# Performance work log

Hardware: AMD Instinct MI355X
Metric: run time of the kernel (lower is better)

Reference implementation:

```python
import jax, jax.numpy as jnp
import numpy as np

W1 = 1.0
W2 = 1.0


def setup_inputs() -> dict:
    key = jax.random.key(0)
    k1, k2 = jax.random.split(key)
    points1 = jax.random.normal(k1, (8, 4096, 3), dtype=jnp.float32)
    points2 = jax.random.normal(k2, (8, 4096, 3), dtype=jnp.float32)
    return {"points1": points1, "points2": points2}


def reference(points1, points2):
    # Pairwise squared L2 distances: [B, N1, N2].
    # (torch code does sqrt(dist)**2 which is mathematically identity for dist>=0.)
    diff = points1[:, :, None, :] - points2[:, None, :, :]  # [B, N1, N2, 3]
    dist = jnp.sum(diff * diff, axis=3)                      # [B, N1, N2]
    dist_min1 = jnp.min(dist, axis=2)  # nearest in points2 for each points1: [B, N1]
    dist_min2 = jnp.min(dist, axis=1)  # nearest in points1 for each points2: [B, N2]
    loss1 = dist_min1.mean(axis=1)     # [B]
    loss2 = dist_min2.mean(axis=1)     # [B]
    loss = W1 * loss1 + W2 * loss2
    return loss.mean()  # each_batch=False
```

## Files before the change

kernel.cpp:

```cpp
#include <hip/hip_runtime.h>
#include <float.h>


typedef float v2f __attribute__((ext_vector_type(2)));

#define NBATCH 8
#define NPTS   4096
#define BLK    256
#define PTS    16
#define NCHUNK 32
#define CHUNK  (NPTS / NCHUNK)
#define PAIRS  (CHUNK / 2)

__global__ __launch_bounds__(BLK)
void chamfer_min_kernel(const float* __restrict__ p1,
                        const float* __restrict__ p2,
                        unsigned int* __restrict__ mins )
{
    __shared__ float4 sXY[PAIRS];
    __shared__ float4 sZW[PAIRS];

    int bid   = blockIdx.x;
    int chunk = bid & (NCHUNK - 1);  bid >>= 5;
    int b     = bid & (NBATCH - 1);  bid >>= 3;
    int dir   = bid;

    const float* A    = dir ? p2 : p1;
    const float* Bpts = dir ? p1 : p2;
    int tid = threadIdx.x;

    if (tid < PAIRS) {
        const float* s = Bpts + ((size_t)b * NPTS + chunk * CHUNK + 2 * tid) * 3;
        float x0 = s[0], y0 = s[1], z0 = s[2];
        float x1 = s[3], y1 = s[4], z1 = s[5];
        sXY[tid] = make_float4(x0, x1, y0, y1);
        sZW[tid] = make_float4(z0, z1,
                               x0 * x0 + y0 * y0 + z0 * z0,
                               x1 * x1 + y1 * y1 + z1 * z1);
    }

    v2f  m2x[PTS], m2y[PTS], m2z[PTS];
    float n1[PTS], bestE[PTS], bestO[PTS];
#pragma unroll
    for (int k = 0; k < PTS; ++k) {
        const float* s = A + ((size_t)b * NPTS + tid + k * BLK) * 3;
        float x = s[0], y = s[1], z = s[2];
        float mx = -2.0f * x, my = -2.0f * y, mz = -2.0f * z;
        m2x[k] = (v2f){mx, mx};
        m2y[k] = (v2f){my, my};
        m2z[k] = (v2f){mz, mz};
        n1[k]  = x * x + y * y + z * z;
        bestE[k] = FLT_MAX;
        bestO[k] = FLT_MAX;
    }
    __syncthreads();

#pragma unroll 2
    for (int p = 0; p < PAIRS; ++p) {
        float4 xy = sXY[p];
        float4 zw = sZW[p];
        v2f qx = (v2f){xy.x, xy.y};
        v2f qy = (v2f){xy.z, xy.w};
        v2f qz = (v2f){zw.x, zw.y};
        v2f qw = (v2f){zw.z, zw.w};
#pragma unroll
        for (int k = 0; k < PTS; ++k) {
            v2f t = __builtin_elementwise_fma(m2x[k], qx, qw);
            t = __builtin_elementwise_fma(m2y[k], qy, t);
            t = __builtin_elementwise_fma(m2z[k], qz, t);
            bestE[k] = fminf(bestE[k], t.x);
            bestO[k] = fminf(bestO[k], t.y);
        }
    }

    unsigned int* marr = mins + ((size_t)dir * NBATCH + b) * NPTS + tid;
#pragma unroll
    for (int k = 0; k < PTS; ++k) {
        float d = fmaxf(fminf(bestE[k], bestO[k]) + n1[k], 0.0f);
        atomicMin(&marr[k * BLK], __float_as_uint(d));
    }
}

__global__ __launch_bounds__(1024)
void chamfer_reduce_kernel(const float* __restrict__ mins, float* __restrict__ out)
{
    __shared__ float wave_sums[16];
    const float4* m4 = (const float4*)mins;
    float s = 0.0f;
#pragma unroll
    for (int i = 0; i < 16; ++i) {
        float4 v = m4[threadIdx.x + i * 1024];
        s += (v.x + v.y) + (v.z + v.w);
    }
#pragma unroll
    for (int off = 32; off > 0; off >>= 1)
        s += __shfl_down(s, off, 64);
    int wave = threadIdx.x >> 6;
    if ((threadIdx.x & 63) == 0) wave_sums[wave] = s;
    __syncthreads();
    if (threadIdx.x < 16) {
        s = wave_sums[threadIdx.x];
#pragma unroll
        for (int off = 8; off > 0; off >>= 1)
            s += __shfl_down(s, off, 16);
        if (threadIdx.x == 0) out[0] = s / (float)(NBATCH * NPTS);
    }
}

extern "C" void kernel_launch(void* const* d_in, const int* in_sizes, int n_in,
                              void* d_out, int out_size, void* d_ws, size_t ws_size,
                              hipStream_t stream) {
    const float* p1 = (const float*)d_in[0];
    const float* p2 = (const float*)d_in[1];
    float* out = (float*)d_out;
    unsigned int* mins = (unsigned int*)d_ws;

    hipMemsetAsync(d_ws, 0xFF, (size_t)2 * NBATCH * NPTS * sizeof(unsigned int), stream);

    int nblocks = 2 * NBATCH * NCHUNK;
    chamfer_min_kernel<<<nblocks, BLK, 0, stream>>>(p1, p2, mins);
    chamfer_reduce_kernel<<<1, 1024, 0, stream>>>((const float*)d_ws, out);
}
```

Measured before the change: 82.38 us.

## Merge even/odd minima and split final reduction into two kernels

Folds the two per-point running minima (even and odd pair lanes) into one accumulator using a nested fminf, which cuts register use in the inner loop. The single-block 1024-thread reduction becomes a 64-block first pass that writes partial sums to workspace, followed by a one-wavefront final kernel. This spreads the reduction's memory reads across more CUs, at the cost of an extra kernel launch. The merged min also lengthens the dependency chain on each accumulator.

```diff
diff --git a/kernel.cpp b/kernel.cpp
--- a/kernel.cpp
+++ b/kernel.cpp
@@ -40,7 +40,7 @@
     }
 
     v2f  m2x[PTS], m2y[PTS], m2z[PTS];
-    float n1[PTS], bestE[PTS], bestO[PTS];
+    float n1[PTS], best[PTS];
 #pragma unroll
     for (int k = 0; k < PTS; ++k) {
         const float* s = A + ((size_t)b * NPTS + tid + k * BLK) * 3;
@@ -50,8 +50,7 @@
         m2y[k] = (v2f){my, my};
         m2z[k] = (v2f){mz, mz};
         n1[k]  = x * x + y * y + z * z;
-        bestE[k] = FLT_MAX;
-        bestO[k] = FLT_MAX;
+        best[k] = FLT_MAX;
     }
     __syncthreads();
 
@@ -68,43 +67,42 @@
             v2f t = __builtin_elementwise_fma(m2x[k], qx, qw);
             t = __builtin_elementwise_fma(m2y[k], qy, t);
             t = __builtin_elementwise_fma(m2z[k], qz, t);
-            bestE[k] = fminf(bestE[k], t.x);
-            bestO[k] = fminf(bestO[k], t.y);
+            best[k] = fminf(fminf(best[k], t.x), t.y);
         }
     }
 
     unsigned int* marr = mins + ((size_t)dir * NBATCH + b) * NPTS + tid;
 #pragma unroll
     for (int k = 0; k < PTS; ++k) {
-        float d = fmaxf(fminf(bestE[k], bestO[k]) + n1[k], 0.0f);
+        float d = fmaxf(best[k] + n1[k], 0.0f);
         atomicMin(&marr[k * BLK], __float_as_uint(d));
     }
 }
 
-__global__ __launch_bounds__(1024)
-void chamfer_reduce_kernel(const float* __restrict__ mins, float* __restrict__ out)
+__global__ __launch_bounds__(256)
+void chamfer_reduce1(const float* __restrict__ mins, float* __restrict__ partials)
 {
-    __shared__ float wave_sums[16];
-    const float4* m4 = (const float4*)mins;
-    float s = 0.0f;
-#pragma unroll
-    for (int i = 0; i < 16; ++i) {
-        float4 v = m4[threadIdx.x + i * 1024];
-        s += (v.x + v.y) + (v.z + v.w);
-    }
+    __shared__ float wave_sums[4];
+    int idx = blockIdx.x * 256 + threadIdx.x;
+    float4 v = ((const float4*)mins)[idx];
+    float s = (v.x + v.y) + (v.z + v.w);
 #pragma unroll
     for (int off = 32; off > 0; off >>= 1)
         s += __shfl_down(s, off, 64);
-    int wave = threadIdx.x >> 6;
-    if ((threadIdx.x & 63) == 0) wave_sums[wave] = s;
+    if ((threadIdx.x & 63) == 0) wave_sums[threadIdx.x >> 6] = s;
     __syncthreads();
-    if (threadIdx.x < 16) {
-        s = wave_sums[threadIdx.x];
+    if (threadIdx.x == 0)
+        partials[blockIdx.x] = (wave_sums[0] + wave_sums[1]) + (wave_sums[2] + wave_sums[3]);
+}
+
+__global__ __launch_bounds__(64)
+void chamfer_reduce2(const float* __restrict__ partials, float* __restrict__ out)
+{
+    float s = partials[threadIdx.x];
 #pragma unroll
-        for (int off = 8; off > 0; off >>= 1)
-            s += __shfl_down(s, off, 16);
-        if (threadIdx.x == 0) out[0] = s / (float)(NBATCH * NPTS);
-    }
+    for (int off = 32; off > 0; off >>= 1)
+        s += __shfl_down(s, off, 64);
+    if (threadIdx.x == 0) out[0] = s / (float)(NBATCH * NPTS);
 }
 
 extern "C" void kernel_launch(void* const* d_in, const int* in_sizes, int n_in,
@@ -114,10 +112,12 @@
     const float* p2 = (const float*)d_in[1];
     float* out = (float*)d_out;
     unsigned int* mins = (unsigned int*)d_ws;
+    float* partials = (float*)d_ws + 2 * NBATCH * NPTS;
 
     hipMemsetAsync(d_ws, 0xFF, (size_t)2 * NBATCH * NPTS * sizeof(unsigned int), stream);
 
     int nblocks = 2 * NBATCH * NCHUNK;
     chamfer_min_kernel<<<nblocks, BLK, 0, stream>>>(p1, p2, mins);
-    chamfer_reduce_kernel<<<1, 1024, 0, stream>>>((const float*)d_ws, out);
+    chamfer_reduce1<<<64, 256, 0, stream>>>((const float*)d_ws, partials);
+    chamfer_reduce2<<<1, 64, 0, stream>>>(partials, out);
 }
```

Result: no change. 81.13 us (-1.5%).
